# Performance work log

Measured on AMD Instinct MI355X. Metric: run time of the kernel, lower is better.

The kernel has to match this reference:

```python
import jax, jax.numpy as jnp
import numpy as np

N_NODES = 100000
N_EDGES = 3200000
N_F = 128
HIDDEN = 128
N_PRED = 8
K_HOPS = 3
N_GRAPHS = 64


def setup_inputs() -> dict:
    key = jax.random.key(0)
    k1, k2, k3, k4, k5, k6, k7, k8 = jax.random.split(key, 8)
    x = jax.random.normal(k1, (N_NODES, N_F), dtype=jnp.float32)
    edge_index = jax.random.randint(k2, (2, N_EDGES), 0, N_NODES, dtype=jnp.int64)
    edge_attr = jax.random.uniform(k3, (N_EDGES,), dtype=jnp.float32)
    batch = jnp.sort(jax.random.randint(k4, (N_NODES,), 0, N_GRAPHS, dtype=jnp.int64))
    # SGConv internal Linear: in=n_f, out=hidden (applied after K propagations)
    s1 = 1.0 / np.sqrt(N_F)
    W_conv = jax.random.uniform(k5, (HIDDEN, N_F), dtype=jnp.float32, minval=-s1, maxval=s1)
    b_conv = jax.random.uniform(k6, (HIDDEN,), dtype=jnp.float32, minval=-s1, maxval=s1)
    s2 = 1.0 / np.sqrt(HIDDEN)
    W_lin = jax.random.uniform(k7, (N_PRED, HIDDEN), dtype=jnp.float32, minval=-s2, maxval=s2)
    b_lin = jax.random.uniform(k8, (N_PRED,), dtype=jnp.float32, minval=-s2, maxval=s2)
    return {"x": x, "edge_index": edge_index, "edge_attr": edge_attr, "batch": batch,
            "W_conv": W_conv, "b_conv": b_conv, "W_lin": W_lin, "b_lin": b_lin}


def _gcn_norm(edge_index, edge_weight, num_nodes):
    # Add self-loops with weight 1 (PyG gcn_norm default), then symmetric normalize.
    loop = jnp.arange(num_nodes, dtype=edge_index.dtype)
    row = jnp.concatenate([edge_index[0], loop])
    col = jnp.concatenate([edge_index[1], loop])
    w = jnp.concatenate([edge_weight, jnp.ones((num_nodes,), dtype=edge_weight.dtype)])
    deg = jax.ops.segment_sum(w, col, num_segments=num_nodes)
    dinv = jnp.where(deg > 0, jax.lax.rsqrt(jnp.where(deg > 0, deg, 1.0)), 0.0)
    norm = dinv[row] * w * dinv[col]
    return row, col, norm


def reference(x, edge_index, edge_attr, batch, W_conv, b_conv, W_lin, b_lin):
    N = x.shape[0]
    row, col, norm = _gcn_norm(edge_index, edge_attr, N)
    h = x
    for _ in range(K_HOPS):  # K repeated gather-scale-scatter propagations
        h = jax.ops.segment_sum(norm[:, None] * h[row], col, num_segments=N)
    h = h @ W_conv.T + b_conv  # SGConv linear: [N, hidden]
    # global_mean_pool by batch id
    sums = jax.ops.segment_sum(h, batch, num_segments=N_GRAPHS)
    cnt = jax.ops.segment_sum(jnp.ones((N,), dtype=h.dtype), batch, num_segments=N_GRAPHS)
    pooled = sums / jnp.maximum(cnt, 1.0)[:, None]
    # dropout(p=0.5) is identity in eval mode
    return pooled @ W_lin.T + b_lin
```

## Files before the change

### kernel.cpp

```cpp
#include <hip/hip_runtime.h>

#define NN 100000
#define NE 3200000
#define NF 128
#define NH 128
#define NP 8
#define NG 64

#define CS 10000
#define NC 10
#define NW 64
#define ES (NE / NW)

#define PT 64
#define GP 1024

#define SCAN_B 1024
#define SCAN_NBLK 98

__device__ __forceinline__ unsigned short f2bf(float f) {
    unsigned u = __float_as_uint(f);
    return (unsigned short)((u + 0x7fffu + ((u >> 16) & 1u)) >> 16);
}
__device__ __forceinline__ float bf2f(unsigned short b) {
    return __uint_as_float((unsigned)b << 16);
}

__global__ void k_init(float* __restrict__ cnt, float* __restrict__ psum) {
    int i = blockIdx.x * blockDim.x + threadIdx.x;
    if (i < NG) cnt[i] = 0.0f;
    if (i < NG * NH) psum[i] = 0.0f;
}

__global__ __launch_bounds__(256) void k_hist(const int* __restrict__ row,
                                              unsigned* __restrict__ H) {
    __shared__ unsigned hist[CS];
    int w = blockIdx.x % NW, c = blockIdx.x / NW;
    int rbase = c * CS;
    int nb = (rbase + CS <= NN) ? CS : (NN - rbase);
    for (int i = threadIdx.x; i < nb; i += 256) hist[i] = 0u;
    __syncthreads();
    const int4* r4 = (const int4*)(row + (size_t)w * ES);
    for (int i = threadIdx.x; i < ES / 8; i += 256) {
        int4 a = r4[2 * i], b = r4[2 * i + 1];
        int rs[8] = {a.x, a.y, a.z, a.w, b.x, b.y, b.z, b.w};
#pragma unroll
        for (int j = 0; j < 8; ++j) {
            unsigned rr = (unsigned)(rs[j] - rbase);
            if (rr < (unsigned)nb) atomicAdd(&hist[rr], 1u);
        }
    }
    __syncthreads();
    for (int i = threadIdx.x; i < nb; i += 256) H[(size_t)w * NN + rbase + i] = hist[i];
}

__global__ __launch_bounds__(256) void k_deg_hist(const int* __restrict__ col,
                                                  const float* __restrict__ wt,
                                                  float* __restrict__ Hd) {
    __shared__ float dh[CS];
    int w = blockIdx.x % NW, c = blockIdx.x / NW;
    int rbase = c * CS;
    int nb = (rbase + CS <= NN) ? CS : (NN - rbase);
    for (int i = threadIdx.x; i < nb; i += 256) dh[i] = 0.0f;
    __syncthreads();
    const int4*   c4 = (const int4*)(col + (size_t)w * ES);
    const float4* w4 = (const float4*)(wt + (size_t)w * ES);
    for (int i = threadIdx.x; i < ES / 8; i += 256) {
        int4 a = c4[2 * i], b = c4[2 * i + 1];
        float4 wa = w4[2 * i], wb = w4[2 * i + 1];
        int cc[8] = {a.x, a.y, a.z, a.w, b.x, b.y, b.z, b.w};
        float ww[8] = {wa.x, wa.y, wa.z, wa.w, wb.x, wb.y, wb.z, wb.w};
#pragma unroll
        for (int j = 0; j < 8; ++j) {
            unsigned rr = (unsigned)(cc[j] - rbase);
            if (rr < (unsigned)nb) atomicAdd(&dh[rr], ww[j]);
        }
    }
    __syncthreads();
    for (int i = threadIdx.x; i < nb; i += 256) Hd[(size_t)w * NN + rbase + i] = dh[i];
}

__global__ void k_cnt(const int* __restrict__ batch, float* __restrict__ cnt) {
    __shared__ float c[NG];
    int t = threadIdx.x;
    if (t < NG) c[t] = 0.0f;
    __syncthreads();
    int i = blockIdx.x * blockDim.x + t;
    if (i < NN) atomicAdd(&c[batch[i]], 1.0f);
    __syncthreads();
    if (t < NG && c[t] != 0.0f) atomicAdd(&cnt[t], c[t]);
}

__global__ void k_reduce(const unsigned* __restrict__ H, const float* __restrict__ Hd,
                         int* __restrict__ rcnt, float* __restrict__ dinv) {
    int r = blockIdx.x * blockDim.x + threadIdx.x;
    if (r >= NN) return;
    unsigned s = 0;
    float d = 1.0f;
#pragma unroll
    for (int w = 0; w < NW; ++w) {
        s += H[(size_t)w * NN + r];
        d += Hd[(size_t)w * NN + r];
    }
    rcnt[r] = (int)s;
    dinv[r] = rsqrtf(d);
}

__global__ __launch_bounds__(SCAN_B) void k_scan1(const int* __restrict__ rcnt,
                                                  int* __restrict__ px,
                                                  int* __restrict__ bsum) {
    __shared__ int s[SCAN_B];
    int t = threadIdx.x;
    int i = blockIdx.x * SCAN_B + t;
    int v = (i < NN) ? rcnt[i] : 0;
    s[t] = v;
    __syncthreads();
    for (int off = 1; off < SCAN_B; off <<= 1) {
        int x = (t >= off) ? s[t - off] : 0;
        __syncthreads();
        s[t] += x;
        __syncthreads();
    }
    px[i] = s[t] - v;
    if (t == SCAN_B - 1) bsum[blockIdx.x] = s[t];
}

__global__ void k_scan2(const int* __restrict__ bsum, int* __restrict__ bofs) {
    if (threadIdx.x == 0) {
        int acc = 0;
        for (int b = 0; b < SCAN_NBLK; ++b) { bofs[b] = acc; acc += bsum[b]; }
    }
}

__global__ void k_scan3(const int* __restrict__ px, const int* __restrict__ bofs,
                        int* __restrict__ rowptr) {
    int i = blockIdx.x * blockDim.x + threadIdx.x;
    if (i > NN) return;
    rowptr[i] = px[i] + bofs[i >> 10];
}

__global__ void k_base(const int* __restrict__ rowptr, unsigned* __restrict__ H) {
    int r = blockIdx.x * blockDim.x + threadIdx.x;
    if (r >= NN) return;
    unsigned acc = (unsigned)rowptr[r];
#pragma unroll
    for (int w = 0; w < NW; ++w) {
        unsigned v = H[(size_t)w * NN + r];
        H[(size_t)w * NN + r] = acc;
        acc += v;
    }
}

__global__ __launch_bounds__(256) void k_sort(const int* __restrict__ row,
                                              const int* __restrict__ col,
                                              const float* __restrict__ wt,
                                              const unsigned* __restrict__ B,
                                              const float* __restrict__ dinv,
                                              float2* __restrict__ pack) {
    __shared__ unsigned basel[CS];
    int w = blockIdx.x % NW, c = blockIdx.x / NW;
    int rbase = c * CS;
    int nb = (rbase + CS <= NN) ? CS : (NN - rbase);
    for (int i = threadIdx.x; i < nb; i += 256)
        basel[i] = B[(size_t)w * NN + rbase + i];
    __syncthreads();
    const int4*   r4 = (const int4*)(row + (size_t)w * ES);
    const int4*   c4 = (const int4*)(col + (size_t)w * ES);
    const float4* w4 = (const float4*)(wt + (size_t)w * ES);
    for (int i = threadIdx.x; i < ES / 8; i += 256) {
        int4 ra = r4[2 * i], rb = r4[2 * i + 1];
        int4 ca = c4[2 * i], cb = c4[2 * i + 1];
        float4 wa = w4[2 * i], wb = w4[2 * i + 1];
        int rs[8] = {ra.x, ra.y, ra.z, ra.w, rb.x, rb.y, rb.z, rb.w};
        int cs[8] = {ca.x, ca.y, ca.z, ca.w, cb.x, cb.y, cb.z, cb.w};
        float ww[8] = {wa.x, wa.y, wa.z, wa.w, wb.x, wb.y, wb.z, wb.w};
#pragma unroll
        for (int j = 0; j < 8; ++j) {
            unsigned rr = (unsigned)(rs[j] - rbase);
            if (rr < (unsigned)nb) {
                unsigned pos = atomicAdd(&basel[rr], 1u);
                pack[pos] = make_float2(__int_as_float(cs[j]),
                                        dinv[rs[j]] * ww[j] * dinv[cs[j]]);
            }
        }
    }
}

__device__ __forceinline__ void pk_nt(const float2* __restrict__ pack, int idx,
                                      int& cc, float& w) {
    unsigned long long pu =
        __builtin_nontemporal_load((const unsigned long long*)pack + idx);
    cc = (int)(unsigned)pu;
    w = __uint_as_float((unsigned)(pu >> 32));
}

__global__ void k_q1_gather(const int* __restrict__ rowptr, const float2* __restrict__ pack,
                            const int* __restrict__ batch, const float* __restrict__ dinv,
                            unsigned short* __restrict__ Q) {
    int wid = (blockIdx.x * blockDim.x + threadIdx.x) >> 6;
    int lane = threadIdx.x & 63;
    if (wid >= NN) return;
    int es = lane >> 3;
    int gg = lane & 7;
    int beg = rowptr[wid], end = rowptr[wid + 1];
    float d = dinv[wid];
    int bself = batch[wid];
    float dd = d * d;
    float acc[8];
#pragma unroll
    for (int i = 0; i < 8; ++i)
        acc[i] = (es == 0 && bself == gg * 8 + i) ? dd : 0.0f;

    if (beg < end) {
        int last = end - 1;
        for (int e = beg; e < end; e += 32) {
            int i0 = e + es, i1 = e + 8 + es, i2 = e + 16 + es, i3 = e + 24 + es;
            int c0, c1, c2, c3; float w0, w1, w2, w3;
            pk_nt(pack, min(i0, last), c0, w0);
            pk_nt(pack, min(i1, last), c1, w1);
            pk_nt(pack, min(i2, last), c2, w2);
            pk_nt(pack, min(i3, last), c3, w3);
            if (i0 > last) w0 = 0.0f;
            if (i1 > last) w1 = 0.0f;
            if (i2 > last) w2 = 0.0f;
            if (i3 > last) w3 = 0.0f;
            int b0 = batch[c0];
            int b1 = batch[c1];
            int b2 = batch[c2];
            int b3 = batch[c3];
#pragma unroll
            for (int i = 0; i < 8; ++i) {
                int g = gg * 8 + i;
                acc[i] += (b0 == g) ? w0 : 0.0f;
                acc[i] += (b1 == g) ? w1 : 0.0f;
                acc[i] += (b2 == g) ? w2 : 0.0f;
                acc[i] += (b3 == g) ? w3 : 0.0f;
            }
        }
    }
#pragma unroll
    for (int m = 8; m <= 32; m <<= 1)
#pragma unroll
        for (int i = 0; i < 8; ++i) acc[i] += __shfl_xor(acc[i], m, 64);
    if (es == 0) {
        uint4 o;
        o.x = (unsigned)f2bf(acc[0]) | ((unsigned)f2bf(acc[1]) << 16);
        o.y = (unsigned)f2bf(acc[2]) | ((unsigned)f2bf(acc[3]) << 16);
        o.z = (unsigned)f2bf(acc[4]) | ((unsigned)f2bf(acc[5]) << 16);
        o.w = (unsigned)f2bf(acc[6]) | ((unsigned)f2bf(acc[7]) << 16);
        ((uint4*)Q)[(size_t)wid * 8 + gg] = o;
    }
}

__global__ void k_hop_gather(const int* __restrict__ rowptr, const float2* __restrict__ pack,
                             const float* __restrict__ dinv,
                             const unsigned short* __restrict__ Qin,
                             unsigned short* __restrict__ Qout) {
    int wid = (blockIdx.x * blockDim.x + threadIdx.x) >> 6;
    int lane = threadIdx.x & 63;
    if (wid >= NN) return;
    int es = lane >> 3;
    int gg = lane & 7;
    int beg = rowptr[wid], end = rowptr[wid + 1];
    float d = dinv[wid];
    const uint4* Q4 = (const uint4*)Qin;

    float acc[8];
    if (es == 0) {
        uint4 qs = Q4[(size_t)wid * 8 + gg];
        float dd = d * d;
        acc[0] = dd * __uint_as_float(qs.x << 16);
        acc[1] = dd * __uint_as_float(qs.x & 0xffff0000u);
        acc[2] = dd * __uint_as_float(qs.y << 16);
        acc[3] = dd * __uint_as_float(qs.y & 0xffff0000u);
        acc[4] = dd * __uint_as_float(qs.z << 16);
        acc[5] = dd * __uint_as_float(qs.z & 0xffff0000u);
        acc[6] = dd * __uint_as_float(qs.w << 16);
        acc[7] = dd * __uint_as_float(qs.w & 0xffff0000u);
    } else {
#pragma unroll
        for (int i = 0; i < 8; ++i) acc[i] = 0.0f;
    }

    if (beg < end) {
        int last = end - 1;
        for (int e = beg; e < end; e += 32) {
            int i0 = e + es, i1 = e + 8 + es, i2 = e + 16 + es, i3 = e + 24 + es;
            int c0, c1, c2, c3; float w0, w1, w2, w3;
            pk_nt(pack, min(i0, last), c0, w0);
            pk_nt(pack, min(i1, last), c1, w1);
            pk_nt(pack, min(i2, last), c2, w2);
            pk_nt(pack, min(i3, last), c3, w3);
            if (i0 > last) w0 = 0.0f;
            if (i1 > last) w1 = 0.0f;
            if (i2 > last) w2 = 0.0f;
            if (i3 > last) w3 = 0.0f;
            uint4 q0 = Q4[(size_t)c0 * 8 + gg];
            uint4 q1 = Q4[(size_t)c1 * 8 + gg];
            uint4 q2 = Q4[(size_t)c2 * 8 + gg];
            uint4 q3 = Q4[(size_t)c3 * 8 + gg];
            acc[0] += w0 * __uint_as_float(q0.x << 16);
            acc[1] += w0 * __uint_as_float(q0.x & 0xffff0000u);
            acc[2] += w0 * __uint_as_float(q0.y << 16);
            acc[3] += w0 * __uint_as_float(q0.y & 0xffff0000u);
            acc[4] += w0 * __uint_as_float(q0.z << 16);
            acc[5] += w0 * __uint_as_float(q0.z & 0xffff0000u);
            acc[6] += w0 * __uint_as_float(q0.w << 16);
            acc[7] += w0 * __uint_as_float(q0.w & 0xffff0000u);
            acc[0] += w1 * __uint_as_float(q1.x << 16);
            acc[1] += w1 * __uint_as_float(q1.x & 0xffff0000u);
            acc[2] += w1 * __uint_as_float(q1.y << 16);
            acc[3] += w1 * __uint_as_float(q1.y & 0xffff0000u);
            acc[4] += w1 * __uint_as_float(q1.z << 16);
            acc[5] += w1 * __uint_as_float(q1.z & 0xffff0000u);
            acc[6] += w1 * __uint_as_float(q1.w << 16);
            acc[7] += w1 * __uint_as_float(q1.w & 0xffff0000u);
            acc[0] += w2 * __uint_as_float(q2.x << 16);
            acc[1] += w2 * __uint_as_float(q2.x & 0xffff0000u);
            acc[2] += w2 * __uint_as_float(q2.y << 16);
            acc[3] += w2 * __uint_as_float(q2.y & 0xffff0000u);
            acc[4] += w2 * __uint_as_float(q2.z << 16);
            acc[5] += w2 * __uint_as_float(q2.z & 0xffff0000u);
            acc[6] += w2 * __uint_as_float(q2.w << 16);
            acc[7] += w2 * __uint_as_float(q2.w & 0xffff0000u);
            acc[0] += w3 * __uint_as_float(q3.x << 16);
            acc[1] += w3 * __uint_as_float(q3.x & 0xffff0000u);
            acc[2] += w3 * __uint_as_float(q3.y << 16);
            acc[3] += w3 * __uint_as_float(q3.y & 0xffff0000u);
            acc[4] += w3 * __uint_as_float(q3.z << 16);
            acc[5] += w3 * __uint_as_float(q3.z & 0xffff0000u);
            acc[6] += w3 * __uint_as_float(q3.w << 16);
            acc[7] += w3 * __uint_as_float(q3.w & 0xffff0000u);
        }
    }
#pragma unroll
    for (int m = 8; m <= 32; m <<= 1)
#pragma unroll
        for (int i = 0; i < 8; ++i) acc[i] += __shfl_xor(acc[i], m, 64);
    if (es == 0) {
        uint4 o;
        o.x = (unsigned)f2bf(acc[0]) | ((unsigned)f2bf(acc[1]) << 16);
        o.y = (unsigned)f2bf(acc[2]) | ((unsigned)f2bf(acc[3]) << 16);
        o.z = (unsigned)f2bf(acc[4]) | ((unsigned)f2bf(acc[5]) << 16);
        o.w = (unsigned)f2bf(acc[6]) | ((unsigned)f2bf(acc[7]) << 16);
        ((uint4*)Qout)[(size_t)wid * 8 + gg] = o;
    }
}

__global__ __launch_bounds__(256) void k_pool(const unsigned short* __restrict__ Q,
                                              const float* __restrict__ x,
                                              float* __restrict__ partial) {
    __shared__ unsigned short qsh[PT * NG];
    __shared__ float xs[PT * NF];
    int t = threadIdx.x;
    int f4 = (t & 31) << 2;
    int g0 = (t >> 5) << 3;
    float4 acc[8];
#pragma unroll
    for (int i = 0; i < 8; ++i) acc[i] = make_float4(0.f, 0.f, 0.f, 0.f);

    const int NT = (NN + PT - 1) / PT;
    for (int tile = blockIdx.x; tile < NT; tile += GP) {
        int n0 = tile * PT;
        int nt = min(PT, NN - n0);
        const uint4*  Q4 = (const uint4*)(Q + (size_t)n0 * NG);
        const float4* X4 = (const float4*)(x + (size_t)n0 * NF);
        uint4*  qs4 = (uint4*)qsh;
        float4* xs4 = (float4*)xs;
        for (int i = t; i < nt * (NG / 8); i += 256) qs4[i] = Q4[i];
        for (int i = t; i < nt * (NF / 4); i += 256) xs4[i] = X4[i];
        __syncthreads();
        for (int n = 0; n < nt; ++n) {
            float4 xv = *(const float4*)&xs[n * NF + f4];
            uint4 qu = *(const uint4*)&qsh[n * NG + g0];
            float qv[8];
            qv[0] = __uint_as_float(qu.x << 16);
            qv[1] = __uint_as_float(qu.x & 0xffff0000u);
            qv[2] = __uint_as_float(qu.y << 16);
            qv[3] = __uint_as_float(qu.y & 0xffff0000u);
            qv[4] = __uint_as_float(qu.z << 16);
            qv[5] = __uint_as_float(qu.z & 0xffff0000u);
            qv[6] = __uint_as_float(qu.w << 16);
            qv[7] = __uint_as_float(qu.w & 0xffff0000u);
#pragma unroll
            for (int i = 0; i < 8; ++i) {
                acc[i].x += qv[i] * xv.x;
                acc[i].y += qv[i] * xv.y;
                acc[i].z += qv[i] * xv.z;
                acc[i].w += qv[i] * xv.w;
            }
        }
        __syncthreads();
    }
    float* pb = partial + (size_t)blockIdx.x * (NG * NF);
#pragma unroll
    for (int i = 0; i < 8; ++i)
        *(float4*)&pb[(g0 + i) * NF + f4] = acc[i];
}

__global__ void k_red(const float* __restrict__ partial, float* __restrict__ psum) {
    int gid = blockIdx.x * blockDim.x + threadIdx.x;
    int idx = gid & (NG * NF - 1);
    int j = gid >> 13;
    float acc = 0.0f;
    for (int b = j; b < GP; b += 8)
        acc += partial[(size_t)b * (NG * NF) + idx];
    atomicAdd(&psum[idx], acc);
}

__global__ void k_final(const float* __restrict__ psum, const float* __restrict__ cnt,
                        const float* __restrict__ Wc, const float* __restrict__ bc,
                        const float* __restrict__ Wl, const float* __restrict__ bl,
                        float* __restrict__ out) {
    __shared__ float M[NP * NH];
    __shared__ float bias[NP];
    int t = threadIdx.x;
    for (int idx = t; idx < NP * NH; idx += 256) {
        int p = idx >> 7, f = idx & 127;
        float s = 0.0f;
        for (int h = 0; h < NH; ++h) s += Wl[p * NH + h] * Wc[h * NF + f];
        M[idx] = s;
    }
    if (t < NP) {
        float s = bl[t];
        for (int h = 0; h < NH; ++h) s += Wl[t * NH + h] * bc[h];
        bias[t] = s;
    }
    __syncthreads();
    for (int idx = t; idx < NG * NP; idx += 256) {
        int g = idx >> 3, p = idx & 7;
        float inv = 1.0f / fmaxf(cnt[g], 1.0f);
        float s = 0.0f;
        for (int f = 0; f < NF; ++f) s += psum[g * NF + f] * M[p * NH + f];
        out[idx] = s * inv + bias[p];
    }
}

extern "C" void kernel_launch(void* const* d_in, const int* in_sizes, int n_in,
                              void* d_out, int out_size, void* d_ws, size_t ws_size,
                              hipStream_t stream) {
    const float* x     = (const float*)d_in[0];
    const int*   ei    = (const int*)d_in[1];
    const float* ea    = (const float*)d_in[2];
    const int*   batch = (const int*)d_in[3];
    const float* Wc    = (const float*)d_in[4];
    const float* bc    = (const float*)d_in[5];
    const float* Wl    = (const float*)d_in[6];
    const float* bl    = (const float*)d_in[7];
    const int* row = ei;
    const int* col = ei + NE;
    float* out = (float*)d_out;

    float* ws     = (float*)d_ws;
    float*  dinv   = ws;
    int*    rowptr = (int*)(dinv + NN);
    float*  cnt    = (float*)(rowptr + NN + 4);
    float*  psum   = cnt + NG;
    float2* pack   = (float2*)(psum + NG * NH);
    unsigned* H    = (unsigned*)(pack + NE);
    float*    Hd   = (float*)(H + (size_t)NW * NN);
    unsigned short* Qa = (unsigned short*)H;
    unsigned short* Qb = Qa + (size_t)NN * NG;
    float* partial = (float*)Qb;
    int* rcnt = (int*)pack;
    int* px   = rcnt + SCAN_NBLK * SCAN_B;
    int* bsum = px + SCAN_NBLK * SCAN_B;
    int* bofs = bsum + SCAN_NBLK;

    const int B = 256;
    int gN  = (NN + B - 1) / B;
    int gCW = NC * NW;
    int gW  = (int)(((long long)NN * 64 + B - 1) / B);

    k_init<<<(NG * NH + B - 1) / B, B, 0, stream>>>(cnt, psum);
    k_hist<<<gCW, B, 0, stream>>>(row, H);
    k_deg_hist<<<gCW, B, 0, stream>>>(col, ea, Hd);
    k_cnt<<<gN, B, 0, stream>>>(batch, cnt);
    k_reduce<<<gN, B, 0, stream>>>(H, Hd, rcnt, dinv);

    k_scan1<<<SCAN_NBLK, SCAN_B, 0, stream>>>(rcnt, px, bsum);
    k_scan2<<<1, 64, 0, stream>>>(bsum, bofs);
    k_scan3<<<(NN + 1 + SCAN_B - 1) / SCAN_B, SCAN_B, 0, stream>>>(px, bofs, rowptr);
    k_base<<<gN, B, 0, stream>>>(rowptr, H);
    k_sort<<<gCW, B, 0, stream>>>(row, col, ea, H, dinv, pack);

    k_q1_gather<<<gW, B, 0, stream>>>(rowptr, pack, batch, dinv, Qa);
    k_hop_gather<<<gW, B, 0, stream>>>(rowptr, pack, dinv, Qa, Qb);
    k_hop_gather<<<gW, B, 0, stream>>>(rowptr, pack, dinv, Qb, Qa);

    k_pool<<<GP, B, 0, stream>>>(Qa, x, partial);
    k_red<<<256, B, 0, stream>>>(partial, psum);
    k_final<<<1, B, 0, stream>>>(psum, cnt, Wc, bc, Wl, bl, out);
}
```

Measured before the change: 609.4 us.

## Replace chunked shared-memory CSR histogram and sort with single-pass global atomics

The old CSR build split nodes into 10 shared-memory chunks and scanned the edge lists once per chunk in each of the histogram, degree and sort kernels, plus per-slice reduce and base passes. The new build reads each edge once: one pass does global atomic row counts and degree sums, and a second pass scatters edges into the packed array through a per-row atomic cursor set up during the scan. This removes the repeated edge reads and the 64-slice histogram traffic. In exchange it adds contention on global atomics, and edges within a row land in a nondeterministic order, so float summation order can vary between runs.

```diff
diff --git a/kernel.cpp b/kernel.cpp
--- a/kernel.cpp
+++ b/kernel.cpp
@@ -7,11 +7,6 @@
 #define NP 8
 #define NG 64
 
-#define CS 10000
-#define NC 10
-#define NW 64
-#define ES (NE / NW)
-
 #define PT 64
 #define GP 1024
 
@@ -26,58 +21,35 @@
     return __uint_as_float((unsigned)b << 16);
 }
 
-__global__ void k_init(float* __restrict__ cnt, float* __restrict__ psum) {
+__global__ void k_init(float* __restrict__ cnt, float* __restrict__ psum,
+                       int* __restrict__ rcnt, float* __restrict__ deg) {
     int i = blockIdx.x * blockDim.x + threadIdx.x;
     if (i < NG) cnt[i] = 0.0f;
     if (i < NG * NH) psum[i] = 0.0f;
-}
-
-__global__ __launch_bounds__(256) void k_hist(const int* __restrict__ row,
-                                              unsigned* __restrict__ H) {
-    __shared__ unsigned hist[CS];
-    int w = blockIdx.x % NW, c = blockIdx.x / NW;
-    int rbase = c * CS;
-    int nb = (rbase + CS <= NN) ? CS : (NN - rbase);
-    for (int i = threadIdx.x; i < nb; i += 256) hist[i] = 0u;
-    __syncthreads();
-    const int4* r4 = (const int4*)(row + (size_t)w * ES);
-    for (int i = threadIdx.x; i < ES / 8; i += 256) {
-        int4 a = r4[2 * i], b = r4[2 * i + 1];
-        int rs[8] = {a.x, a.y, a.z, a.w, b.x, b.y, b.z, b.w};
-#pragma unroll
-        for (int j = 0; j < 8; ++j) {
-            unsigned rr = (unsigned)(rs[j] - rbase);
-            if (rr < (unsigned)nb) atomicAdd(&hist[rr], 1u);
-        }
-    }
-    __syncthreads();
-    for (int i = threadIdx.x; i < nb; i += 256) H[(size_t)w * NN + rbase + i] = hist[i];
-}
-
-__global__ __launch_bounds__(256) void k_deg_hist(const int* __restrict__ col,
-                                                  const float* __restrict__ wt,
-                                                  float* __restrict__ Hd) {
-    __shared__ float dh[CS];
-    int w = blockIdx.x % NW, c = blockIdx.x / NW;
-    int rbase = c * CS;
-    int nb = (rbase + CS <= NN) ? CS : (NN - rbase);
-    for (int i = threadIdx.x; i < nb; i += 256) dh[i] = 0.0f;
-    __syncthreads();
-    const int4*   c4 = (const int4*)(col + (size_t)w * ES);
-    const float4* w4 = (const float4*)(wt + (size_t)w * ES);
-    for (int i = threadIdx.x; i < ES / 8; i += 256) {
-        int4 a = c4[2 * i], b = c4[2 * i + 1];
-        float4 wa = w4[2 * i], wb = w4[2 * i + 1];
-        int cc[8] = {a.x, a.y, a.z, a.w, b.x, b.y, b.z, b.w};
-        float ww[8] = {wa.x, wa.y, wa.z, wa.w, wb.x, wb.y, wb.z, wb.w};
-#pragma unroll
-        for (int j = 0; j < 8; ++j) {
-            unsigned rr = (unsigned)(cc[j] - rbase);
-            if (rr < (unsigned)nb) atomicAdd(&dh[rr], ww[j]);
-        }
-    }
-    __syncthreads();
-    for (int i = threadIdx.x; i < nb; i += 256) Hd[(size_t)w * NN + rbase + i] = dh[i];
+    if (i < NN) { rcnt[i] = 0; deg[i] = 0.0f; }
+}
+
+__global__ __launch_bounds__(256) void k_deg2(const int* __restrict__ row,
+                                              const int* __restrict__ col,
+                                              const float* __restrict__ wt,
+                                              int* __restrict__ rcnt,
+                                              float* __restrict__ deg) {
+    int i = blockIdx.x * blockDim.x + threadIdx.x;
+    if (i >= NE / 8) return;
+    const int4*   r4 = (const int4*)row;
+    const int4*   c4 = (const int4*)col;
+    const float4* w4 = (const float4*)wt;
+    int4 ra = r4[2 * i], rb = r4[2 * i + 1];
+    int4 ca = c4[2 * i], cb = c4[2 * i + 1];
+    float4 wa = w4[2 * i], wb = w4[2 * i + 1];
+    int rs[8] = {ra.x, ra.y, ra.z, ra.w, rb.x, rb.y, rb.z, rb.w};
+    int cs[8] = {ca.x, ca.y, ca.z, ca.w, cb.x, cb.y, cb.z, cb.w};
+    float ww[8] = {wa.x, wa.y, wa.z, wa.w, wb.x, wb.y, wb.z, wb.w};
+#pragma unroll
+    for (int j = 0; j < 8; ++j) {
+        atomicAdd(&rcnt[rs[j]], 1);
+        atomicAdd(&deg[cs[j]], ww[j]);
+    }
 }
 
 __global__ void k_cnt(const int* __restrict__ batch, float* __restrict__ cnt) {
@@ -91,19 +63,9 @@
     if (t < NG && c[t] != 0.0f) atomicAdd(&cnt[t], c[t]);
 }
 
-__global__ void k_reduce(const unsigned* __restrict__ H, const float* __restrict__ Hd,
-                         int* __restrict__ rcnt, float* __restrict__ dinv) {
+__global__ void k_dinv(const float* __restrict__ deg, float* __restrict__ dinv) {
     int r = blockIdx.x * blockDim.x + threadIdx.x;
-    if (r >= NN) return;
-    unsigned s = 0;
-    float d = 1.0f;
-#pragma unroll
-    for (int w = 0; w < NW; ++w) {
-        s += H[(size_t)w * NN + r];
-        d += Hd[(size_t)w * NN + r];
-    }
-    rcnt[r] = (int)s;
-    dinv[r] = rsqrtf(d);
+    if (r < NN) dinv[r] = rsqrtf(1.0f + deg[r]);
 }
 
 __global__ __launch_bounds__(SCAN_B) void k_scan1(const int* __restrict__ rcnt,
@@ -133,56 +95,36 @@
 }
 
 __global__ void k_scan3(const int* __restrict__ px, const int* __restrict__ bofs,
-                        int* __restrict__ rowptr) {
+                        int* __restrict__ rowptr, int* __restrict__ cursor) {
     int i = blockIdx.x * blockDim.x + threadIdx.x;
     if (i > NN) return;
-    rowptr[i] = px[i] + bofs[i >> 10];
-}
-
-__global__ void k_base(const int* __restrict__ rowptr, unsigned* __restrict__ H) {
-    int r = blockIdx.x * blockDim.x + threadIdx.x;
-    if (r >= NN) return;
-    unsigned acc = (unsigned)rowptr[r];
-#pragma unroll
-    for (int w = 0; w < NW; ++w) {
-        unsigned v = H[(size_t)w * NN + r];
-        H[(size_t)w * NN + r] = acc;
-        acc += v;
-    }
-}
-
-__global__ __launch_bounds__(256) void k_sort(const int* __restrict__ row,
-                                              const int* __restrict__ col,
-                                              const float* __restrict__ wt,
-                                              const unsigned* __restrict__ B,
-                                              const float* __restrict__ dinv,
-                                              float2* __restrict__ pack) {
-    __shared__ unsigned basel[CS];
-    int w = blockIdx.x % NW, c = blockIdx.x / NW;
-    int rbase = c * CS;
-    int nb = (rbase + CS <= NN) ? CS : (NN - rbase);
-    for (int i = threadIdx.x; i < nb; i += 256)
-        basel[i] = B[(size_t)w * NN + rbase + i];
-    __syncthreads();
-    const int4*   r4 = (const int4*)(row + (size_t)w * ES);
-    const int4*   c4 = (const int4*)(col + (size_t)w * ES);
-    const float4* w4 = (const float4*)(wt + (size_t)w * ES);
-    for (int i = threadIdx.x; i < ES / 8; i += 256) {
-        int4 ra = r4[2 * i], rb = r4[2 * i + 1];
-        int4 ca = c4[2 * i], cb = c4[2 * i + 1];
-        float4 wa = w4[2 * i], wb = w4[2 * i + 1];
-        int rs[8] = {ra.x, ra.y, ra.z, ra.w, rb.x, rb.y, rb.z, rb.w};
-        int cs[8] = {ca.x, ca.y, ca.z, ca.w, cb.x, cb.y, cb.z, cb.w};
-        float ww[8] = {wa.x, wa.y, wa.z, wa.w, wb.x, wb.y, wb.z, wb.w};
-#pragma unroll
-        for (int j = 0; j < 8; ++j) {
-            unsigned rr = (unsigned)(rs[j] - rbase);
-            if (rr < (unsigned)nb) {
-                unsigned pos = atomicAdd(&basel[rr], 1u);
-                pack[pos] = make_float2(__int_as_float(cs[j]),
-                                        dinv[rs[j]] * ww[j] * dinv[cs[j]]);
-            }
-        }
+    int v = px[i] + bofs[i >> 10];
+    rowptr[i] = v;
+    if (i < NN) cursor[i] = v;
+}
+
+__global__ __launch_bounds__(256) void k_sort2(const int* __restrict__ row,
+                                               const int* __restrict__ col,
+                                               const float* __restrict__ wt,
+                                               int* __restrict__ cursor,
+                                               const float* __restrict__ dinv,
+                                               float2* __restrict__ pack) {
+    int i = blockIdx.x * blockDim.x + threadIdx.x;
+    if (i >= NE / 8) return;
+    const int4*   r4 = (const int4*)row;
+    const int4*   c4 = (const int4*)col;
+    const float4* w4 = (const float4*)wt;
+    int4 ra = r4[2 * i], rb = r4[2 * i + 1];
+    int4 ca = c4[2 * i], cb = c4[2 * i + 1];
+    float4 wa = w4[2 * i], wb = w4[2 * i + 1];
+    int rs[8] = {ra.x, ra.y, ra.z, ra.w, rb.x, rb.y, rb.z, rb.w};
+    int cs[8] = {ca.x, ca.y, ca.z, ca.w, cb.x, cb.y, cb.z, cb.w};
+    float ww[8] = {wa.x, wa.y, wa.z, wa.w, wb.x, wb.y, wb.z, wb.w};
+#pragma unroll
+    for (int j = 0; j < 8; ++j) {
+        int pos = atomicAdd(&cursor[rs[j]], 1);
+        pack[pos] = make_float2(__int_as_float(cs[j]),
+                                dinv[rs[j]] * ww[j] * dinv[cs[j]]);
     }
 }
 
@@ -458,31 +400,30 @@
     float*  psum   = cnt + NG;
     float2* pack   = (float2*)(psum + NG * NH);
     unsigned* H    = (unsigned*)(pack + NE);
-    float*    Hd   = (float*)(H + (size_t)NW * NN);
     unsigned short* Qa = (unsigned short*)H;
     unsigned short* Qb = Qa + (size_t)NN * NG;
     float* partial = (float*)Qb;
-    int* rcnt = (int*)pack;
-    int* px   = rcnt + SCAN_NBLK * SCAN_B;
-    int* bsum = px + SCAN_NBLK * SCAN_B;
-    int* bofs = bsum + SCAN_NBLK;
+    int*   rcnt = (int*)pack;
+    int*   px   = rcnt + SCAN_NBLK * SCAN_B;
+    int*   bsum = px + SCAN_NBLK * SCAN_B;
+    int*   bofs = bsum + SCAN_NBLK;
+    float* deg  = (float*)(bofs + SCAN_NBLK);
+    int*   cursor = (int*)H;
 
     const int B = 256;
     int gN  = (NN + B - 1) / B;
-    int gCW = NC * NW;
+    int gE  = (NE / 8 + B - 1) / B;
     int gW  = (int)(((long long)NN * 64 + B - 1) / B);
 
-    k_init<<<(NG * NH + B - 1) / B, B, 0, stream>>>(cnt, psum);
-    k_hist<<<gCW, B, 0, stream>>>(row, H);
-    k_deg_hist<<<gCW, B, 0, stream>>>(col, ea, Hd);
+    k_init<<<gN, B, 0, stream>>>(cnt, psum, rcnt, deg);
+    k_deg2<<<gE, B, 0, stream>>>(row, col, ea, rcnt, deg);
     k_cnt<<<gN, B, 0, stream>>>(batch, cnt);
-    k_reduce<<<gN, B, 0, stream>>>(H, Hd, rcnt, dinv);
+    k_dinv<<<gN, B, 0, stream>>>(deg, dinv);
 
     k_scan1<<<SCAN_NBLK, SCAN_B, 0, stream>>>(rcnt, px, bsum);
     k_scan2<<<1, 64, 0, stream>>>(bsum, bofs);
-    k_scan3<<<(NN + 1 + SCAN_B - 1) / SCAN_B, SCAN_B, 0, stream>>>(px, bofs, rowptr);
-    k_base<<<gN, B, 0, stream>>>(rowptr, H);
-    k_sort<<<gCW, B, 0, stream>>>(row, col, ea, H, dinv, pack);
+    k_scan3<<<(NN + 1 + SCAN_B - 1) / SCAN_B, SCAN_B, 0, stream>>>(px, bofs, rowptr, cursor);
+    k_sort2<<<gE, B, 0, stream>>>(row, col, ea, cursor, dinv, pack);
 
     k_q1_gather<<<gW, B, 0, stream>>>(rowptr, pack, batch, dinv, Qa);
     k_hop_gather<<<gW, B, 0, stream>>>(rowptr, pack, dinv, Qa, Qb);
```

After: 884.2 us. 1.45x slower.
